# Performance work log

Measured on AMD Instinct MI355X. Metric: run time of the kernel, lower is better.

The kernel has to match this reference:

```python
import jax, jax.numpy as jnp
import numpy as np

VOCAB = 34004
EMB = 300
UNITS = 512


def setup_inputs() -> dict:
    key = jax.random.key(0)
    ks = jax.random.split(key, 16)
    s = 0.05
    B, T_in, T_out = 64, 60, 31
    inp = {
        "dec_input": jax.random.randint(ks[0], (B, T_out), 0, VOCAB, dtype=jnp.int64 if jax.config.jax_enable_x64 else jnp.int32),
        "h0": jax.random.normal(ks[1], (B, UNITS), jnp.float32),
        "c0": jax.random.normal(ks[2], (B, UNITS), jnp.float32),
        "memory": jax.random.normal(ks[3], (B, T_in, UNITS), jnp.float32),
        # embedding table
        "embedding": jax.random.normal(ks[4], (VOCAB, EMB), jnp.float32) * s,
        # LSTM cell: input = concat(emb, prev_attention) -> EMB + UNITS
        "Wk": jax.random.normal(ks[5], (EMB + UNITS, 4 * UNITS), jnp.float32) * s,
        "Uk": jax.random.normal(ks[6], (UNITS, 4 * UNITS), jnp.float32) * s,
        "bk": jnp.zeros((4 * UNITS,), jnp.float32),
        # Bahdanau attention: memory layer, query layer, score vector v
        "Wm": jax.random.normal(ks[7], (UNITS, UNITS), jnp.float32) * s,
        "Wq": jax.random.normal(ks[8], (UNITS, UNITS), jnp.float32) * s,
        "v_att": jax.random.normal(ks[9], (UNITS,), jnp.float32) * s,
        # attention_layer (Dense(dec_units, use_bias=False)) on concat(cell_out, context)
        "Wa": jax.random.normal(ks[10], (2 * UNITS, UNITS), jnp.float32) * s,
        # output projection fc to vocab
        "Wfc": jax.random.normal(ks[11], (UNITS, VOCAB), jnp.float32) * s,
        "bfc": jnp.zeros((VOCAB,), jnp.float32),
    }
    return inp


def reference(dec_input, h0, c0, memory, embedding, Wk, Uk, bk, Wm, Wq, v_att, Wa, Wfc, bfc):
    # Teacher-forced (training=True) AttentionWrapper decode with Bahdanau attention.
    keys = jnp.einsum("btd,de->bte", memory, Wm)  # precompute memory projection [B,T_in,U]
    emb = embedding[dec_input]                      # [B,T_out,EMB]
    emb_t = jnp.swapaxes(emb, 0, 1)                 # [T_out,B,EMB]
    attn0 = jnp.zeros_like(h0)                      # initial attention is zeros

    def step(carry, e):
        h, c, attn = carry
        x = jnp.concatenate([e, attn], axis=-1)     # default cell_input_fn: concat
        z = x @ Wk + h @ Uk + bk                    # [B,4U]
        i, f, g, o = jnp.split(z, 4, axis=-1)       # keras LSTM gate order i,f,c,o
        i = jax.nn.sigmoid(i); f = jax.nn.sigmoid(f)
        g = jnp.tanh(g); o = jax.nn.sigmoid(o)
        c_new = f * c + i * g
        h_new = o * jnp.tanh(c_new)
        # Bahdanau score: v^T tanh(W_m*memory + W_q*query)
        q = h_new @ Wq                               # [B,U]
        score = jnp.einsum("btu,u->bt", jnp.tanh(keys + q[:, None, :]), v_att)
        align = jax.nn.softmax(score, axis=-1)       # [B,T_in]
        context = jnp.einsum("bt,btd->bd", align, memory)
        attn_new = jnp.concatenate([h_new, context], axis=-1) @ Wa  # attention_layer
        logits = attn_new @ Wfc + bfc                # output_layer (fc)
        return (h_new, c_new, attn_new), logits

    _, logits = jax.lax.scan(step, (h0, c0, attn0), emb_t)
    return jnp.swapaxes(logits, 0, 1)               # [B, T_out, vocab] = rnn_output
```

## Files before the change

### kernel.cpp

```cpp
#include <hip/hip_runtime.h>
#include <cstdint>
#include <cstddef>

typedef _Float16 f16;
typedef _Float16 f16x8 __attribute__((ext_vector_type(8)));
typedef float    f32x4 __attribute__((ext_vector_type(4)));
typedef uint32_t u32x4 __attribute__((ext_vector_type(4)));

#define DEV static __device__ __forceinline__

constexpr int TOUT = 31;
constexpr int VOC  = 34004;
constexpr int VOCP = 34048;

constexpr size_t OFF_SYNC  = 0;
constexpr size_t OFF_MEM16 = 8192;
constexpr size_t OFF_WMSWZ = OFF_MEM16 + (size_t)3840*512*2;
constexpr size_t OFF_KEYS  = OFF_WMSWZ + (size_t)16*512*32*2;
constexpr size_t OFF_EMBA  = OFF_KEYS  + (size_t)3840*512*2;
constexpr size_t OFF_WKTOP = OFF_EMBA  + (size_t)1984*320*2;
constexpr size_t OFF_EMBW  = OFF_WKTOP + (size_t)10*2048*32*2;
constexpr size_t OFF_WA16  = OFF_EMBW  + (size_t)1984*2048*4;
constexpr size_t OFF_WKATT = OFF_WA16  + (size_t)1024*512*2;
constexpr size_t OFF_WCA   = OFF_WKATT + (size_t)16*2048*32*2;
constexpr size_t OFF_WSTAR = OFF_WCA   + (size_t)1024*2048*4;
constexpr size_t OFF_UK16  = OFF_WSTAR + (size_t)32*2048*32*2;
constexpr size_t OFF_WQSWZ = OFF_UK16  + (size_t)16*2048*32*2;
constexpr size_t OFF_WASWZ = OFF_WQSWZ + (size_t)512*512*2;
constexpr size_t OFF_H016  = OFF_WASWZ + (size_t)32*512*32*2;
constexpr size_t OFF_YALL  = OFF_H016  + (size_t)64*512*2;
constexpr size_t OFF_ATT16 = OFF_YALL  + (size_t)31*64*1024*2;
constexpr size_t OFF_BKP   = OFF_ATT16 + (size_t)1984*512*2;
constexpr size_t OFF_WFC   = OFF_BKP   + 8192;
constexpr size_t OFF_QP    = OFF_EMBA;

DEV void gload16(const void* src, void* ldsbase ) {
  __builtin_amdgcn_global_load_lds(
      (const __attribute__((address_space(1))) unsigned int*)src,
      (__attribute__((address_space(3))) unsigned int*)ldsbase, 16, 0, 0);
}

DEV float sigm(float x)      { return 1.f / (1.f + expf(-x)); }
DEV float tanh_fast(float x) { float e = __expf(2.f*x); return 1.f - 2.f/(e+1.f); }

DEV uint32_t aload_u32(const uint32_t* p){ return __hip_atomic_load(p, __ATOMIC_RELAXED, __HIP_MEMORY_SCOPE_AGENT); }
DEV void astore_u32(uint32_t* p, uint32_t v){ __hip_atomic_store(p, v, __ATOMIC_RELAXED, __HIP_MEMORY_SCOPE_AGENT); }

DEV void ld16_sc1(const void* p, u32x4& d){
  asm volatile("global_load_dwordx4 %0, %1, off sc1" : "=v"(d) : "v"(p));
}
DEV void st16_sc1(void* p, u32x4 v){
  asm volatile("global_store_dwordx4 %0, %1, off sc1" :: "v"(p), "v"(v) : "memory");
}
DEV void vwait(){ asm volatile("s_waitcnt vmcnt(0)" ::: "memory"); }

__global__ void prep_elem(char* ws, const int* dec, const float* h0,
                          const float* memory, const float* embt,
                          const float* Wa, const float* bk)
{
  f16* mem16 = (f16*)(ws+OFF_MEM16);
  f16* embA  = (f16*)(ws+OFF_EMBA);
  f16* wa16  = (f16*)(ws+OFF_WA16);
  f16* h016  = (f16*)(ws+OFF_H016);
  float* bkp = (float*)(ws+OFF_BKP);
  constexpr int E0=1966080, E1=E0+634880, E2=E1+524288, E3=E2+32768, E4=E3+2048;
  for (int i = blockIdx.x*256 + threadIdx.x; i < E4; i += gridDim.x*256) {
    if (i < E0) { mem16[i] = (f16)memory[i]; }
    else if (i < E1) { int j=i-E0; int r=j/320, k=j-r*320; int t=r>>6, b=r&63;
      int tok = dec[b*TOUT+t];
      embA[j] = (k<300) ? (f16)embt[(size_t)tok*300+k] : (f16)0.f; }
    else if (i < E2) { int j=i-E1; wa16[j] = (f16)Wa[j]; }
    else if (i < E3) { int j=i-E2; h016[j] = (f16)h0[j]; }
    else { int j=i-E3; bkp[j] = bk[(j>>2) + (j&3)*512]; }
  }
}

__global__ void prep_swz(char* ws, const float* Wm, const float* Wk, const float* Uk,
                         const float* Wa, const float* Wq)
{
  int tg = blockIdx.x*256 + threadIdx.x;
  constexpr int S0=8192, S1=S0+20480, S2=S1+32768, S3=S2+32768, S4=S3+16384, S5=S4+8192;
  if (tg >= S5) return;
  f16 buf[32];
  f16* dst;
  if (tg < S0) {
    int kt=tg>>9, n=tg&511;
    #pragma unroll
    for (int kk=0;kk<32;kk++) buf[kk] = (f16)Wm[(size_t)(kt*32+kk)*512 + n];
    dst = (f16*)(ws+OFF_WMSWZ) + (size_t)tg*32;
  } else if (tg < S1) {
    int j=tg-S0; int kt=j>>11, np=j&2047; int col=(np>>2)+(np&3)*512;
    #pragma unroll
    for (int kk=0;kk<32;kk++){ int k=kt*32+kk;
      buf[kk] = (k<300) ? (f16)Wk[(size_t)k*2048+col] : (f16)0.f; }
    dst = (f16*)(ws+OFF_WKTOP) + (size_t)j*32;
  } else if (tg < S2) {
    int j=tg-S1; int kt=j>>11, np=j&2047; int col=(np>>2)+(np&3)*512;
    #pragma unroll
    for (int kk=0;kk<32;kk++) buf[kk] = (f16)Wk[(size_t)(300+kt*32+kk)*2048+col];
    dst = (f16*)(ws+OFF_WKATT) + (size_t)j*32;
  } else if (tg < S3) {
    int j=tg-S2; int kt=j>>11, np=j&2047; int col=(np>>2)+(np&3)*512;
    #pragma unroll
    for (int kk=0;kk<32;kk++) buf[kk] = (f16)Uk[(size_t)(kt*32+kk)*2048+col];
    dst = (f16*)(ws+OFF_UK16) + (size_t)j*32;
  } else if (tg < S4) {
    int j=tg-S3; int kt=j>>9, n=j&511;
    #pragma unroll
    for (int kk=0;kk<32;kk++) buf[kk] = (f16)Wa[(size_t)(kt*32+kk)*512 + n];
    dst = (f16*)(ws+OFF_WASWZ) + (size_t)j*32;
  } else {
    int j=tg-S4; int rr=j>>9, n=j&511;
    #pragma unroll
    for (int kk=0;kk<32;kk++) buf[kk] = (f16)Wq[(size_t)(rr*32+kk)*512 + n];
    dst = (f16*)(ws+OFF_WQSWZ) + (size_t)j*32;
  }
  f16x8* d8 = (f16x8*)dst; f16x8* s8 = (f16x8*)buf;
  d8[0]=s8[0]; d8[1]=s8[1]; d8[2]=s8[2]; d8[3]=s8[3];
}

__global__ void build_wstar(char* ws, const float* Uk)
{
  int tg = blockIdx.x*256 + threadIdx.x;
  int kt = tg>>11, np = tg&2047;
  int col = (np>>2)+(np&3)*512;
  const float* wca = (const float*)(ws+OFF_WCA);
  f16 buf[32];
  #pragma unroll
  for (int kk=0;kk<32;kk++){
    int k = kt*32+kk;
    float v = wca[(size_t)k*2048 + np];
    if (k < 512) v += Uk[(size_t)k*2048 + col];
    buf[kk] = (f16)v;
  }
  f16* dst = (f16*)(ws+OFF_WSTAR) + (size_t)tg*32;
  f16x8* d8 = (f16x8*)dst; f16x8* s8 = (f16x8*)buf;
  d8[0]=s8[0]; d8[1]=s8[1]; d8[2]=s8[2]; d8[3]=s8[3];
}

template<int BM, int BN, int WR, int WC, int MODE>
__global__ __launch_bounds__(WR*WC*64, 1)
void gemm16(const f16* __restrict__ A, int lda,
            const f16* __restrict__ Bs, int Np,
            void* __restrict__ C, const float* __restrict__ bias,
            int M, int K, int Mreal, int Nreal)
{
  constexpr int NT  = WR*WC*64;
  constexpr int WTM = BM/WR, WTN = BN/WC, AM = WTM/16, AN = WTN/16;
  constexpr int NLA = BM*64/(NT*16), NLB = BN*64/(NT*16);
  __shared__ __align__(16) f16 sA[BM*32];
  __shared__ __align__(16) f16 sB[BN*32];
  const int tid = threadIdx.x, wave = tid>>6, lane = tid&63;
  const int lg = lane>>4, lr = lane&15;
  const int m0 = blockIdx.y*BM, n0 = blockIdx.x*BN;
  const int wm = (wave/WC)*WTM, wn = (wave%WC)*WTN;

  f32x4 acc[AM][AN] = {};

  int aoff[AM], boff[AN];
  #pragma unroll
  for (int i=0;i<AM;i++){ int row = wm+i*16+lr; aoff[i] = row*64 + (((lg + (row>>1))&3)<<4); }
  #pragma unroll
  for (int i=0;i<AN;i++){ int row = wn+i*16+lr; boff[i] = row*64 + (((lg + (row>>1))&3)<<4); }

  const int ksteps = K/32;
  for (int ks=0; ks<ksteps; ks++){
    const int k0 = ks*32;
    __syncthreads();
    #pragma unroll
    for (int i=0;i<NLA;i++){
      int p = i*NT + tid;
      int row = p>>2; int g = ((p&3) - (row>>1)) & 3;
      int gm = m0+row; if (gm > Mreal-1) gm = Mreal-1;
      gload16(A + (size_t)gm*lda + k0 + g*8, (char*)sA + (i*NT + wave*64)*16);
    }
    #pragma unroll
    for (int i=0;i<NLB;i++){
      int p = i*NT + tid;
      int row = p>>2; int g = ((p&3) - (row>>1)) & 3;
      gload16(Bs + ((size_t)(k0>>5)*Np + (n0+row))*32 + g*8, (char*)sB + (i*NT + wave*64)*16);
    }
    __syncthreads();
    f16x8 af[AM], bf[AN];
    #pragma unroll
    for (int i=0;i<AM;i++) af[i] = *(const f16x8*)((const char*)sA + aoff[i]);
    #pragma unroll
    for (int i=0;i<AN;i++) bf[i] = *(const f16x8*)((const char*)sB + boff[i]);
    #pragma unroll
    for (int i=0;i<AM;i++)
      #pragma unroll
      for (int j=0;j<AN;j++)
        acc[i][j] = __builtin_amdgcn_mfma_f32_16x16x32_f16(af[i], bf[j], acc[i][j], 0,0,0);
  }

  #pragma unroll
  for (int i=0;i<AM;i++)
    #pragma unroll
    for (int j=0;j<AN;j++){
      int n = n0 + wn + j*16 + lr;
      if (MODE == 2 && n >= Nreal) continue;
      float bb = 0.f;
      if (MODE != 1 && bias) bb = bias[n];
      #pragma unroll
      for (int r=0;r<4;r++){
        int m = m0 + wm + i*16 + lg*4 + r;
        if (m >= Mreal) continue;
        float v = acc[i][j][r] + bb;
        if (MODE == 0)      ((float*)C)[(size_t)m*Np + n] = v;
        else if (MODE == 1) ((f16*)C)[(size_t)m*Np + n] = (f16)v;
        else { int t = m>>6, b = m&63; ((float*)C)[((size_t)(b*TOUT+t))*VOC + n] = v; }
      }
    }
}

DEV void cbar(uint32_t* flags, int cbase, int r, int tid, uint32_t target)
{
  vwait();
  __syncthreads();
  if (tid == 0)
    astore_u32(flags + (size_t)(cbase + r)*32, target);
  if (tid < 16) {
    while (aload_u32(flags + (size_t)(cbase + tid)*32) < target)
      __builtin_amdgcn_s_sleep(1);
  }
  __syncthreads();
}

template<int KS>
DEV f32x4 p1_mfma(const f16* __restrict__ Bs, const char* ylb, int col, int kg, int lr)
{
  f16x8 B[8];
  #pragma unroll
  for (int i=0;i<8;i++)
    B[i] = *(const f16x8*)(Bs + (((size_t)i*2048 + col)<<5) + kg*8);
  f32x4 acc = {};
  #pragma unroll
  for (int ks=0; ks<KS; ks+=8) {
    #pragma unroll
    for (int i=0;i<8;i++) {
      f16x8 a = *(const f16x8*)(ylb + lr*2064 + (ks+i)*64 + kg*16);
      acc = __builtin_amdgcn_mfma_f32_16x16x32_f16(a, B[i], acc, 0,0,0);
      int nk = ks+8+i;
      if (nk < KS)
        B[i] = *(const f16x8*)(Bs + (((size_t)nk*2048 + col)<<5) + kg*8);
    }
  }
  return acc;
}

__global__ __launch_bounds__(512, 1)
void recur_wfc(char* ws, const float* __restrict__ c0, const float* __restrict__ v_att,
               const float* __restrict__ Wfc)
{
  const int blk = blockIdx.x, tid = threadIdx.x;

  if (blk >= 64) {
    const int cb = blk - 64;
    const int n = cb*256 + (tid & 255);
    const int kt0 = (tid >> 8) * 8;
    if (n < VOCP) {
      f16* wdst = (f16*)(ws+OFF_WFC);
      for (int kt = kt0; kt < kt0+8; kt++) {
        f16 buf[32];
        #pragma unroll
        for (int kk=0;kk<32;kk++)
          buf[kk] = (n < VOC) ? (f16)Wfc[(size_t)(kt*32+kk)*VOC + n] : (f16)0.f;
        f16x8* d8 = (f16x8*)((f16*)wdst + ((size_t)kt*VOCP + n)*32);
        f16x8* s8 = (f16x8*)buf;
        d8[0]=s8[0]; d8[1]=s8[1]; d8[2]=s8[2]; d8[3]=s8[3];
      }
    }
    return;
  }

  const int wave = tid>>6, lane = tid&63;
  const int lr = lane&15, kg = lane>>4;
  const int clus = blk>>4, r = blk&15;
  const int cbase = clus<<4;
  const int bown = cbase + r;
  const int n0 = r*128;

  uint32_t* flags = (uint32_t*)(ws+OFF_SYNC);
  char* qpg = (char*)(ws+OFF_QP);
  const f16* wstar = (const f16*)(ws+OFF_WSTAR);
  const f16* uk16  = (const f16*)(ws+OFF_UK16);
  const f16* wqswz = (const f16*)(ws+OFF_WQSWZ);
  const f16* keys16= (const f16*)(ws+OFF_KEYS);
  const f16* mem16 = (const f16*)(ws+OFF_MEM16);
  const float* embw= (const float*)(ws+OFF_EMBW);

  __shared__ __align__(16) char  ybuf[33024];
  __shared__ __align__(16) float zl[16*132];
  __shared__ __align__(16) float c_sl[512];
  __shared__ __align__(16) f16   h_sl[512];
  __shared__ __align__(16) float q_l[512];
  __shared__ __align__(16) float v_l[512];
  __shared__ __align__(16) f16   cx16_l[512];
  __shared__ __align__(16) float sc_l[64];
  __shared__ __align__(16) f16   mem_lds[60*512];

  v_l[tid] = v_att[tid];
  { int b = tid>>5, uu = tid&31;
    c_sl[tid] = c0[(size_t)(cbase+b)*512 + r*32 + uu]; }

  {
    const char* msrc = (const char*)(mem16 + (size_t)bown*60*512);
    #pragma unroll
    for (int i=0;i<8;i++){
      int cb2 = i*512 + wave*64;
      if (cb2 < 3840)
        gload16(msrc + ((size_t)cb2 + lane)*16, (char*)mem_lds + (size_t)cb2*16);
    }
  }

  for (int t=0; t<TOUT; t++){
    {
      const char* ysrc; int rsh;
      if (t == 0) { ysrc = ws+OFF_H016; rsh = 6; }
      else        { ysrc = ws+OFF_YALL + (size_t)(t-1)*64*2048; rsh = 7; }
      const int npass = (16 << rsh) >> 9;
      u32x4 g[4];
      #pragma unroll
      for (int p=0;p<4;p++){
        if (p < npass){
          int cid = p*512 + tid, row = cid>>rsh, off = cid & ((1<<rsh)-1);
          ld16_sc1(ysrc + ((size_t)(cbase+row) << (rsh+4)) + off*16, g[p]);
        }
      }
      vwait();
      #pragma unroll
      for (int p=0;p<4;p++){
        if (p < npass){
          int cid = p*512 + tid, row = cid>>rsh, off = cid & ((1<<rsh)-1);
          *(u32x4*)(ybuf + row*2064 + off*16) = g[p];
        }
      }
      __syncthreads();
    }

    {
      const int col = n0 + wave*16 + lr;
      f32x4 acc = (t==0) ? p1_mfma<16>(uk16,  ybuf, col, kg, lr)
                         : p1_mfma<32>(wstar, ybuf, col, kg, lr);
      #pragma unroll
      for (int rr=0;rr<4;rr++)
        zl[(kg*4+rr)*132 + wave*16 + lr] = acc[rr];
    }
    __syncthreads();

    {
      const int b = tid>>5, uu = tid&31;
      f32x4 zz = *(const f32x4*)(zl + b*132 + uu*4);
      f32x4 e  = *(const f32x4*)(embw + ((size_t)(t*64+cbase+b))*2048 + n0 + uu*4);
      float ig = sigm(zz[0]+e[0]), fg = sigm(zz[1]+e[1]);
      float gg = tanhf(zz[2]+e[2]), og = sigm(zz[3]+e[3]);
      float cn = fg*c_sl[tid] + ig*gg;
      c_sl[tid] = cn;
      h_sl[tid] = (f16)(og * tanhf(cn));
    }
    __syncthreads();

    char* yt = (char*)(ws+OFF_YALL) + (size_t)t*64*2048;
    if (tid < 64){
      int b = tid>>2, off = tid&3;
      u32x4 v = *(const u32x4*)((const char*)h_sl + b*64 + off*16);
      st16_sc1(yt + (size_t)(cbase+b)*2048 + r*64 + off*16, v);
    }

    {
      float* qs = (float*)ybuf;
      f16x8 a = *(const f16x8*)(h_sl + lr*32 + kg*8);
      #pragma unroll
      for (int j=0;j<4;j++){
        int n = wave*64 + j*16 + lr;
        f16x8 bf = *(const f16x8*)(wqswz + ((size_t)(r*512 + n))*32 + kg*8);
        f32x4 aq = __builtin_amdgcn_mfma_f32_16x16x32_f16(a, bf, (f32x4){0.f,0.f,0.f,0.f}, 0,0,0);
        #pragma unroll
        for (int rr=0;rr<4;rr++)
          qs[(kg*4+rr)*512 + n] = aq[rr];
      }
    }
    __syncthreads();
    {
      #pragma unroll
      for (int p=0;p<4;p++){
        int cid = p*512 + tid;
        u32x4 v = *(const u32x4*)(ybuf + cid*16);
        st16_sc1(qpg + (size_t)blk*32768 + cid*16, v);
      }
    }
    cbar(flags, cbase, r, tid, 2*t+1);

    {
      u32x4 gq[4];
      #pragma unroll
      for (int p=0;p<4;p++){
        int cid = p*512 + tid, s = cid>>7, off = cid&127;
        ld16_sc1(qpg + (size_t)(cbase+s)*32768 + r*2048 + off*16, gq[p]);
      }
      vwait();
      #pragma unroll
      for (int p=0;p<4;p++){
        int cid = p*512 + tid;
        *(u32x4*)(ybuf + cid*16) = gq[p];
      }
      __syncthreads();
      const float* qin = (const float*)ybuf;
      float qsum = 0.f;
      #pragma unroll
      for (int s=0;s<16;s++) qsum += qin[s*512 + tid];
      q_l[tid] = qsum;
    }
    __syncthreads();

    for (int i = wave; i < 60; i += 8){
      const f16* krow = keys16 + ((size_t)(bown*60+i))*512;
      float p = 0.f;
      #pragma unroll
      for (int s=0;s<8;s++){
        int u = lane + s*64;
        p += tanh_fast((float)krow[u] + q_l[u]) * v_l[u];
      }
      #pragma unroll
      for (int m=32;m;m>>=1) p += __shfl_xor(p, m, 64);
      if (lane == 0) sc_l[i] = p;
    }
    __syncthreads();
    if (wave == 0){
      float s = (lane < 60) ? sc_l[lane] : -1e30f;
      float mx = s;
      #pragma unroll
      for (int m=32;m;m>>=1) mx = fmaxf(mx, __shfl_xor(mx, m, 64));
      float ev = (lane < 60) ? __expf(s - mx) : 0.f;
      float sum = ev;
      #pragma unroll
      for (int m=32;m;m>>=1) sum += __shfl_xor(sum, m, 64);
      if (lane < 60) sc_l[lane] = ev / sum;
    }
    __syncthreads();
    {
      float cx = 0.f;
      #pragma unroll
      for (int i=0;i<60;i++) cx += sc_l[i] * (float)mem_lds[i*512 + tid];
      cx16_l[tid] = (f16)cx;
    }
    __syncthreads();
    if (tid < 64){
      u32x4 v = *(const u32x4*)((const char*)cx16_l + tid*16);
      st16_sc1(yt + (size_t)bown*2048 + 1024 + tid*16, v);
    }
    cbar(flags, cbase, r, tid, 2*t+2);
  }
}

extern "C" void kernel_launch(void* const* d_in, const int* in_sizes, int n_in,
                              void* d_out, int out_size, void* d_ws, size_t ws_size,
                              hipStream_t stream)
{
  const int*   dec  = (const int*)  d_in[0];
  const float* h0   = (const float*)d_in[1];
  const float* c0   = (const float*)d_in[2];
  const float* mem  = (const float*)d_in[3];
  const float* embt = (const float*)d_in[4];
  const float* Wk   = (const float*)d_in[5];
  const float* Uk   = (const float*)d_in[6];
  const float* bk   = (const float*)d_in[7];
  const float* Wm   = (const float*)d_in[8];
  const float* Wq   = (const float*)d_in[9];
  const float* va   = (const float*)d_in[10];
  const float* Wa   = (const float*)d_in[11];
  const float* Wfc  = (const float*)d_in[12];
  const float* bfc  = (const float*)d_in[13];
  char* ws = (char*)d_ws;

  hipMemsetAsync(ws + OFF_SYNC, 0, 8192, stream);

  prep_elem<<<4096, 256, 0, stream>>>(ws, dec, h0, mem, embt, Wa, bk);
  prep_swz <<<464, 256, 0, stream>>>(ws, Wm, Wk, Uk, Wa, Wq);

  gemm16<128,64,2,2,1><<<dim3(8,30), 256, 0, stream>>>(
      (const f16*)(ws+OFF_MEM16), 512, (const f16*)(ws+OFF_WMSWZ), 512,
      ws+OFF_KEYS, nullptr, 3840, 512, 3840, 512);
  gemm16<128,64,2,2,0><<<dim3(32,16), 256, 0, stream>>>(
      (const f16*)(ws+OFF_EMBA), 320, (const f16*)(ws+OFF_WKTOP), 2048,
      ws+OFF_EMBW, (const float*)(ws+OFF_BKP), 1984, 320, 1984, 2048);
  gemm16<128,64,2,2,0><<<dim3(32,8), 256, 0, stream>>>(
      (const f16*)(ws+OFF_WA16), 512, (const f16*)(ws+OFF_WKATT), 2048,
      ws+OFF_WCA, nullptr, 1024, 512, 1024, 2048);
  build_wstar<<<256, 256, 0, stream>>>(ws, Uk);

  recur_wfc<<<204, 512, 0, stream>>>(ws, c0, va, Wfc);

  gemm16<128,64,2,2,1><<<dim3(8,16), 256, 0, stream>>>(
      (const f16*)(ws+OFF_YALL), 1024, (const f16*)(ws+OFF_WASWZ), 512,
      ws+OFF_ATT16, nullptr, 1984, 1024, 1984, 512);
  gemm16<256,128,4,2,2><<<dim3(266,8), 512, 0, stream>>>(
      (const f16*)(ws+OFF_ATT16), 512, (const f16*)(ws+OFF_WFC), VOCP,
      d_out, bfc, 1984, 512, 1984, VOC);
}
```

Measured before the change: 792.6 us.

## Merge prep kernels and three precompute GEMMs into single launches; enlarge fc tile

Folds the two preprocessing kernels into one launch, with block ranges dispatching to swizzle or elementwise conversion work. The three independent precompute GEMMs (memory keys, embedding-times-Wk, Wa-times-Wk_att) become one grouped GEMM kernel selected by block index. This removes several launch gaps and lets the small GEMMs share the GPU at once. The final vocab projection GEMM also moves to a 512-row M tile with half as many row blocks, which changes occupancy and tail behaviour.

```diff
diff --git a/kernel.cpp b/kernel.cpp
--- a/kernel.cpp
+++ b/kernel.cpp
@@ -54,17 +54,62 @@
 }
 DEV void vwait(){ asm volatile("s_waitcnt vmcnt(0)" ::: "memory"); }
 
-__global__ void prep_elem(char* ws, const int* dec, const float* h0,
-                          const float* memory, const float* embt,
-                          const float* Wa, const float* bk)
-{
+__global__ void prep_all(char* ws, const int* dec, const float* h0, const float* memory,
+                         const float* embt, const float* Wa, const float* bk,
+                         const float* Wm, const float* Wk, const float* Uk, const float* Wq)
+{
+  const int blk = blockIdx.x, tid = threadIdx.x;
+
+  if (blk < 464) {
+    int tg = blk*256 + tid;
+    constexpr int S0=8192, S1=S0+20480, S2=S1+32768, S3=S2+32768, S4=S3+16384, S5=S4+8192;
+    if (tg >= S5) return;
+    f16 buf[32];
+    f16* dst;
+    if (tg < S0) {
+      int kt=tg>>9, n=tg&511;
+      #pragma unroll
+      for (int kk=0;kk<32;kk++) buf[kk] = (f16)Wm[(size_t)(kt*32+kk)*512 + n];
+      dst = (f16*)(ws+OFF_WMSWZ) + (size_t)tg*32;
+    } else if (tg < S1) {
+      int j=tg-S0; int kt=j>>11, np=j&2047; int col=(np>>2)+(np&3)*512;
+      #pragma unroll
+      for (int kk=0;kk<32;kk++){ int k=kt*32+kk;
+        buf[kk] = (k<300) ? (f16)Wk[(size_t)k*2048+col] : (f16)0.f; }
+      dst = (f16*)(ws+OFF_WKTOP) + (size_t)j*32;
+    } else if (tg < S2) {
+      int j=tg-S1; int kt=j>>11, np=j&2047; int col=(np>>2)+(np&3)*512;
+      #pragma unroll
+      for (int kk=0;kk<32;kk++) buf[kk] = (f16)Wk[(size_t)(300+kt*32+kk)*2048+col];
+      dst = (f16*)(ws+OFF_WKATT) + (size_t)j*32;
+    } else if (tg < S3) {
+      int j=tg-S2; int kt=j>>11, np=j&2047; int col=(np>>2)+(np&3)*512;
+      #pragma unroll
+      for (int kk=0;kk<32;kk++) buf[kk] = (f16)Uk[(size_t)(kt*32+kk)*2048+col];
+      dst = (f16*)(ws+OFF_UK16) + (size_t)j*32;
+    } else if (tg < S4) {
+      int j=tg-S3; int kt=j>>9, n=j&511;
+      #pragma unroll
+      for (int kk=0;kk<32;kk++) buf[kk] = (f16)Wa[(size_t)(kt*32+kk)*512 + n];
+      dst = (f16*)(ws+OFF_WASWZ) + (size_t)j*32;
+    } else {
+      int j=tg-S4; int rr=j>>9, n=j&511;
+      #pragma unroll
+      for (int kk=0;kk<32;kk++) buf[kk] = (f16)Wq[(size_t)(rr*32+kk)*512 + n];
+      dst = (f16*)(ws+OFF_WQSWZ) + (size_t)j*32;
+    }
+    f16x8* d8 = (f16x8*)dst; f16x8* s8 = (f16x8*)buf;
+    d8[0]=s8[0]; d8[1]=s8[1]; d8[2]=s8[2]; d8[3]=s8[3];
+    return;
+  }
+
   f16* mem16 = (f16*)(ws+OFF_MEM16);
   f16* embA  = (f16*)(ws+OFF_EMBA);
   f16* wa16  = (f16*)(ws+OFF_WA16);
   f16* h016  = (f16*)(ws+OFF_H016);
   float* bkp = (float*)(ws+OFF_BKP);
   constexpr int E0=1966080, E1=E0+634880, E2=E1+524288, E3=E2+32768, E4=E3+2048;
-  for (int i = blockIdx.x*256 + threadIdx.x; i < E4; i += gridDim.x*256) {
+  for (int i = (blk-464)*256 + tid; i < E4; i += 512*256) {
     if (i < E0) { mem16[i] = (f16)memory[i]; }
     else if (i < E1) { int j=i-E0; int r=j/320, k=j-r*320; int t=r>>6, b=r&63;
       int tok = dec[b*TOUT+t];
@@ -75,48 +120,87 @@
   }
 }
 
-__global__ void prep_swz(char* ws, const float* Wm, const float* Wk, const float* Uk,
-                         const float* Wa, const float* Wq)
-{
-  int tg = blockIdx.x*256 + threadIdx.x;
-  constexpr int S0=8192, S1=S0+20480, S2=S1+32768, S3=S2+32768, S4=S3+16384, S5=S4+8192;
-  if (tg >= S5) return;
-  f16 buf[32];
-  f16* dst;
-  if (tg < S0) {
-    int kt=tg>>9, n=tg&511;
-    #pragma unroll
-    for (int kk=0;kk<32;kk++) buf[kk] = (f16)Wm[(size_t)(kt*32+kk)*512 + n];
-    dst = (f16*)(ws+OFF_WMSWZ) + (size_t)tg*32;
-  } else if (tg < S1) {
-    int j=tg-S0; int kt=j>>11, np=j&2047; int col=(np>>2)+(np&3)*512;
-    #pragma unroll
-    for (int kk=0;kk<32;kk++){ int k=kt*32+kk;
-      buf[kk] = (k<300) ? (f16)Wk[(size_t)k*2048+col] : (f16)0.f; }
-    dst = (f16*)(ws+OFF_WKTOP) + (size_t)j*32;
-  } else if (tg < S2) {
-    int j=tg-S1; int kt=j>>11, np=j&2047; int col=(np>>2)+(np&3)*512;
-    #pragma unroll
-    for (int kk=0;kk<32;kk++) buf[kk] = (f16)Wk[(size_t)(300+kt*32+kk)*2048+col];
-    dst = (f16*)(ws+OFF_WKATT) + (size_t)j*32;
-  } else if (tg < S3) {
-    int j=tg-S2; int kt=j>>11, np=j&2047; int col=(np>>2)+(np&3)*512;
-    #pragma unroll
-    for (int kk=0;kk<32;kk++) buf[kk] = (f16)Uk[(size_t)(kt*32+kk)*2048+col];
-    dst = (f16*)(ws+OFF_UK16) + (size_t)j*32;
-  } else if (tg < S4) {
-    int j=tg-S3; int kt=j>>9, n=j&511;
-    #pragma unroll
-    for (int kk=0;kk<32;kk++) buf[kk] = (f16)Wa[(size_t)(kt*32+kk)*512 + n];
-    dst = (f16*)(ws+OFF_WASWZ) + (size_t)j*32;
+__global__ __launch_bounds__(256, 1)
+void gemm3(char* ws)
+{
+  constexpr int BM=128, BN=64, NT=256, AM=4, AN=2, NLA=2, NLB=1;
+  __shared__ __align__(16) f16 sA[BM*32];
+  __shared__ __align__(16) f16 sB[BN*32];
+
+  const int blk = blockIdx.x, tid = threadIdx.x;
+  const int wave = tid>>6, lane = tid&63;
+  const int lg = lane>>4, lr = lane&15;
+
+  const f16* A; int lda; const f16* Bs; int Np; void* C; const float* bias = nullptr;
+  int bx, by, K, Mreal, mode;
+  if (blk < 240) {
+    bx = blk & 7; by = blk >> 3;
+    A=(const f16*)(ws+OFF_MEM16); lda=512; Bs=(const f16*)(ws+OFF_WMSWZ); Np=512;
+    C=ws+OFF_KEYS; K=512; Mreal=3840; mode=1;
+  } else if (blk < 752) {
+    int i=blk-240; bx=i&31; by=i>>5;
+    A=(const f16*)(ws+OFF_EMBA); lda=320; Bs=(const f16*)(ws+OFF_WKTOP); Np=2048;
+    C=ws+OFF_EMBW; bias=(const float*)(ws+OFF_BKP); K=320; Mreal=1984; mode=0;
   } else {
-    int j=tg-S4; int rr=j>>9, n=j&511;
-    #pragma unroll
-    for (int kk=0;kk<32;kk++) buf[kk] = (f16)Wq[(size_t)(rr*32+kk)*512 + n];
-    dst = (f16*)(ws+OFF_WQSWZ) + (size_t)j*32;
-  }
-  f16x8* d8 = (f16x8*)dst; f16x8* s8 = (f16x8*)buf;
-  d8[0]=s8[0]; d8[1]=s8[1]; d8[2]=s8[2]; d8[3]=s8[3];
+    int i=blk-752; bx=i&31; by=i>>5;
+    A=(const f16*)(ws+OFF_WA16); lda=512; Bs=(const f16*)(ws+OFF_WKATT); Np=2048;
+    C=ws+OFF_WCA; K=512; Mreal=1024; mode=0;
+  }
+  const int m0 = by*BM, n0 = bx*BN;
+  const int wm = (wave>>1)*64, wn = (wave&1)*32;
+
+  f32x4 acc[AM][AN] = {};
+  int aoff[AM], boff[AN];
+  #pragma unroll
+  for (int i=0;i<AM;i++){ int row = wm+i*16+lr; aoff[i] = row*64 + (((lg + (row>>1))&3)<<4); }
+  #pragma unroll
+  for (int i=0;i<AN;i++){ int row = wn+i*16+lr; boff[i] = row*64 + (((lg + (row>>1))&3)<<4); }
+
+  const int ksteps = K/32;
+  for (int ks=0; ks<ksteps; ks++){
+    const int k0 = ks*32;
+    __syncthreads();
+    #pragma unroll
+    for (int i=0;i<NLA;i++){
+      int p = i*NT + tid;
+      int row = p>>2; int g = ((p&3) - (row>>1)) & 3;
+      int gm = m0+row; if (gm > Mreal-1) gm = Mreal-1;
+      gload16(A + (size_t)gm*lda + k0 + g*8, (char*)sA + (i*NT + wave*64)*16);
+    }
+    #pragma unroll
+    for (int i=0;i<NLB;i++){
+      int p = i*NT + tid;
+      int row = p>>2; int g = ((p&3) - (row>>1)) & 3;
+      gload16(Bs + ((size_t)(k0>>5)*Np + (n0+row))*32 + g*8, (char*)sB + (i*NT + wave*64)*16);
+    }
+    __syncthreads();
+    f16x8 af[AM], bf[AN];
+    #pragma unroll
+    for (int i=0;i<AM;i++) af[i] = *(const f16x8*)((const char*)sA + aoff[i]);
+    #pragma unroll
+    for (int i=0;i<AN;i++) bf[i] = *(const f16x8*)((const char*)sB + boff[i]);
+    #pragma unroll
+    for (int i=0;i<AM;i++)
+      #pragma unroll
+      for (int j=0;j<AN;j++)
+        acc[i][j] = __builtin_amdgcn_mfma_f32_16x16x32_f16(af[i], bf[j], acc[i][j], 0,0,0);
+  }
+
+  #pragma unroll
+  for (int i=0;i<AM;i++)
+    #pragma unroll
+    for (int j=0;j<AN;j++){
+      int n = n0 + wn + j*16 + lr;
+      float bb = (mode == 0 && bias) ? bias[n] : 0.f;
+      #pragma unroll
+      for (int r=0;r<4;r++){
+        int m = m0 + wm + i*16 + lg*4 + r;
+        if (m >= Mreal) continue;
+        float v = acc[i][j][r] + bb;
+        if (mode == 0) ((float*)C)[(size_t)m*Np + n] = v;
+        else           ((f16*)C)[(size_t)m*Np + n] = (f16)v;
+      }
+    }
 }
 
 __global__ void build_wstar(char* ws, const float* Uk)
@@ -475,18 +559,10 @@
 
   hipMemsetAsync(ws + OFF_SYNC, 0, 8192, stream);
 
-  prep_elem<<<4096, 256, 0, stream>>>(ws, dec, h0, mem, embt, Wa, bk);
-  prep_swz <<<464, 256, 0, stream>>>(ws, Wm, Wk, Uk, Wa, Wq);
-
-  gemm16<128,64,2,2,1><<<dim3(8,30), 256, 0, stream>>>(
-      (const f16*)(ws+OFF_MEM16), 512, (const f16*)(ws+OFF_WMSWZ), 512,
-      ws+OFF_KEYS, nullptr, 3840, 512, 3840, 512);
-  gemm16<128,64,2,2,0><<<dim3(32,16), 256, 0, stream>>>(
-      (const f16*)(ws+OFF_EMBA), 320, (const f16*)(ws+OFF_WKTOP), 2048,
-      ws+OFF_EMBW, (const float*)(ws+OFF_BKP), 1984, 320, 1984, 2048);
-  gemm16<128,64,2,2,0><<<dim3(32,8), 256, 0, stream>>>(
-      (const f16*)(ws+OFF_WA16), 512, (const f16*)(ws+OFF_WKATT), 2048,
-      ws+OFF_WCA, nullptr, 1024, 512, 1024, 2048);
+  prep_all<<<976, 256, 0, stream>>>(ws, dec, h0, mem, embt, Wa, bk, Wm, Wk, Uk, Wq);
+
+  gemm3<<<1008, 256, 0, stream>>>(ws);
+
   build_wstar<<<256, 256, 0, stream>>>(ws, Uk);
 
   recur_wfc<<<204, 512, 0, stream>>>(ws, c0, va, Wfc);
@@ -494,7 +570,8 @@
   gemm16<128,64,2,2,1><<<dim3(8,16), 256, 0, stream>>>(
       (const f16*)(ws+OFF_YALL), 1024, (const f16*)(ws+OFF_WASWZ), 512,
       ws+OFF_ATT16, nullptr, 1984, 1024, 1984, 512);
-  gemm16<256,128,4,2,2><<<dim3(266,8), 512, 0, stream>>>(
+
+  gemm16<512,128,4,2,2><<<dim3(266,4), 512, 0, stream>>>(
       (const f16*)(ws+OFF_ATT16), 512, (const f16*)(ws+OFF_WFC), VOCP,
       d_out, bfc, 1984, 512, 1984, VOC);
 }
```

After: 818.8 us. +3.3%, slower.
